# Kernel tuning notes

Hardware: AMD Instinct MI355X
Metric: run time of the kernel (lower is better)

Reference implementation:

```python
import jax, jax.numpy as jnp
import numpy as np

N_HIT = 30000   # hits per plane
N_EDGE = 90000  # Delaunay planar edges per plane (~3N)
N_SP = 30000    # spacepoints
H = 128         # hidden dim
F_IN = 4        # wire, time, integral, rms
N_CLASS = 5     # semantic classes
N_ITERS = 3     # core message-passing iterations
PLANES = ("u", "v", "y")


def setup_inputs() -> dict:
    key = jax.random.key(0)
    ks = iter(jax.random.split(key, 64))
    inp = {}
    for p in PLANES:
        inp[f"x_{p}"] = jax.random.normal(next(ks), (N_HIT, F_IN), jnp.float32)
        inp[f"edge_{p}"] = jax.random.randint(next(ks), (2, N_EDGE), 0, N_HIT)
        # row 0: hit index in plane, row 1: spacepoint index
        inp[f"nexus_{p}"] = jax.random.randint(next(ks), (2, N_SP), 0, N_HIT)
    def lin(k, i, o):
        return (jax.random.normal(k, (i, o), jnp.float32) / np.sqrt(i)).astype(jnp.float32)
    inp["W_enc"] = lin(next(ks), F_IN, H); inp["b_enc"] = jnp.zeros((H,), jnp.float32)
    inp["W_msg1"] = lin(next(ks), 2 * H, H); inp["b_msg1"] = jnp.zeros((H,), jnp.float32)
    inp["W_msg2"] = lin(next(ks), H, H); inp["b_msg2"] = jnp.zeros((H,), jnp.float32)
    inp["W_upd"] = lin(next(ks), 2 * H, H); inp["b_upd"] = jnp.zeros((H,), jnp.float32)
    inp["W_sp"] = lin(next(ks), H, H); inp["b_sp"] = jnp.zeros((H,), jnp.float32)
    inp["W_nx"] = lin(next(ks), 2 * H, H); inp["b_nx"] = jnp.zeros((H,), jnp.float32)
    inp["W_sem"] = lin(next(ks), H, N_CLASS); inp["b_sem"] = jnp.zeros((N_CLASS,), jnp.float32)
    return inp


def _segment_mean(data, ids, num):
    s = jax.ops.segment_sum(data, ids, num_segments=num)
    c = jax.ops.segment_sum(jnp.ones((ids.shape[0],), data.dtype), ids, num_segments=num)
    return s / jnp.maximum(c, 1.0)[:, None]


def _core(hs, edges, nexus, W_msg1, b_msg1, W_msg2, b_msg2, W_upd, b_upd,
          W_sp, b_sp, W_nx, b_nx):
    # --- planar convolution per plane (gather-transform-scatter) ---
    new_hs = []
    for h, e in zip(hs, edges):
        src, dst = e[0], e[1]
        m = jnp.concatenate([h[dst], h[src]], axis=-1)          # [E, 2H]
        m = jax.nn.relu(m @ W_msg1 + b_msg1) @ W_msg2 + b_msg2  # [E, H]
        agg = _segment_mean(m, dst, h.shape[0])                 # [N, H]
        upd = jax.nn.relu(jnp.concatenate([h, agg], -1) @ W_upd + b_upd)
        new_hs.append(h + upd)
    hs = new_hs
    # --- nexus convolution: planes -> spacepoints -> planes ---
    sp = jnp.zeros((N_SP, hs[0].shape[1]), hs[0].dtype)
    for h, nx in zip(hs, nexus):
        sp = sp + _segment_mean(h[nx[0]], nx[1], N_SP)
    sp = jax.nn.relu(sp @ W_sp + b_sp)                          # [N_SP, H]
    out_hs = []
    for h, nx in zip(hs, nexus):
        back = _segment_mean(sp[nx[1]], nx[0], h.shape[0])      # [N, H]
        upd = jax.nn.relu(jnp.concatenate([h, back], -1) @ W_nx + b_nx)
        out_hs.append(h + upd)
    return out_hs


def reference(x_u, x_v, x_y, edge_u, edge_v, edge_y, nexus_u, nexus_v, nexus_y,
              W_enc, b_enc, W_msg1, b_msg1, W_msg2, b_msg2, W_upd, b_upd,
              W_sp, b_sp, W_nx, b_nx, W_sem, b_sem):
    edges = (edge_u, edge_v, edge_y)
    nexus = (nexus_u, nexus_v, nexus_y)
    # encoder
    hs = [jax.nn.relu(x @ W_enc + b_enc) for x in (x_u, x_v, x_y)]
    # core message-passing iterations (planar + nexus)
    for _ in range(N_ITERS):
        hs = _core(hs, edges, nexus, W_msg1, b_msg1, W_msg2, b_msg2,
                   W_upd, b_upd, W_sp, b_sp, W_nx, b_nx)
    # semantic decoder per plane
    return tuple(h @ W_sem + b_sem for h in hs)
```

## Files before the change

### kernel.cpp

```cpp
#include <hip/hip_runtime.h>
#include <hip/hip_fp16.h>

#define N_HITS 30000
#define N_EDGES 90000
#define N_SPS 30000
#define HD 128
#define NCLS 5

#define PADM 136

typedef __attribute__((ext_vector_type(8))) _Float16 f16x8;
typedef __attribute__((ext_vector_type(4))) float floatx4;

__device__ __forceinline__ float2 h2f2(uint u) {
    union { uint u; __half2 h; } x; x.u = u;
    return __half22float2(x.h);
}
__device__ __forceinline__ uint f2h2(float a, float b) {
    union { uint u; __half2 h; } x;
    x.h = __halves2half2(__float2half(a), __float2half(b));
    return x.u;
}

__global__ void hist_all_kernel(const int* __restrict__ eu, const int* __restrict__ ev,
                                const int* __restrict__ ey, const int* __restrict__ nu,
                                const int* __restrict__ nv, const int* __restrict__ ny,
                                int* __restrict__ cnt) {
    int gid = blockIdx.x * blockDim.x + threadIdx.x;
    if (gid >= 450000) return;
    int p = gid / 150000;
    int r = gid - p * 150000;
    const int* e = (p == 0) ? eu : (p == 1) ? ev : ey;
    const int* nx = (p == 0) ? nu : (p == 1) ? nv : ny;
    if (r < N_EDGES) {
        atomicAdd(&cnt[p * 30000 + e[N_EDGES + r]], 1);
    } else if (r < N_EDGES + N_SPS) {
        int i = r - N_EDGES;
        atomicAdd(&cnt[(3 + p) * 30000 + nx[N_SPS + i]], 1);
    } else {
        int i = r - N_EDGES - N_SPS;
        atomicAdd(&cnt[(6 + p) * 30000 + nx[i]], 1);
    }
}

__launch_bounds__(1024)
__global__ void scan_kernel(const int* __restrict__ cnt, int* __restrict__ off,
                            int* __restrict__ cursor) {
    int seg = blockIdx.x;
    const int* c = cnt + seg * 30000;
    int* o = off + seg * 30001;
    int* cur = cursor + seg * 30000;
    int t = threadIdx.x;
    int base = t * 30;
    int lc[30];
    int sum = 0;
#pragma unroll
    for (int k = 0; k < 30; ++k) {
        int i = base + k;
        lc[k] = (i < 30000) ? c[i] : 0;
        sum += lc[k];
    }
    __shared__ int part[1024];
    part[t] = sum;
    __syncthreads();
    for (int d = 1; d < 1024; d <<= 1) {
        int x = (t >= d) ? part[t - d] : 0;
        __syncthreads();
        part[t] += x;
        __syncthreads();
    }
    int run = part[t] - sum;
#pragma unroll
    for (int k = 0; k < 30; ++k) {
        int i = base + k;
        if (i < 30000) { o[i] = run; cur[i] = run; run += lc[k]; }
    }
    if (t == 1023) o[30000] = part[1023];
}

__global__ void fill_kernel(const int* __restrict__ eu, const int* __restrict__ ev,
                            const int* __restrict__ ey, const int* __restrict__ nu,
                            const int* __restrict__ nv, const int* __restrict__ ny,
                            int* __restrict__ cursor, int* __restrict__ csr_e,
                            int* __restrict__ csr_s, int* __restrict__ csr_h) {
    int gid = blockIdx.x * blockDim.x + threadIdx.x;
    if (gid >= 450000) return;
    int p = gid / 150000;
    int r = gid - p * 150000;
    const int* e = (p == 0) ? eu : (p == 1) ? ev : ey;
    const int* nx = (p == 0) ? nu : (p == 1) ? nv : ny;
    if (r < N_EDGES) {
        int d = e[N_EDGES + r];
        int pos = atomicAdd(&cursor[p * 30000 + d], 1);
        csr_e[p * N_EDGES + pos] = e[r];
    } else if (r < N_EDGES + N_SPS) {
        int i = r - N_EDGES;
        int spid = nx[N_SPS + i];
        int pos = atomicAdd(&cursor[(3 + p) * 30000 + spid], 1);
        csr_s[p * N_SPS + pos] = nx[i];
    } else {
        int i = r - N_EDGES - N_SPS;
        int hit = nx[i];
        int pos = atomicAdd(&cursor[(6 + p) * 30000 + hit], 1);
        csr_h[p * N_SPS + pos] = nx[N_SPS + i];
    }
}

__device__ __forceinline__ void pack4(const float* __restrict__ W, _Float16* __restrict__ P,
                                      int idx, int koff) {
    int j = idx & 7, lane = (idx >> 3) & 63, ks = (idx >> 9) & 3, n = (idx >> 11) & 7;
    int k = ks * 32 + (lane >> 4) * 8 + j, col = n * 16 + (lane & 15);
    P[idx] = (_Float16)W[(k + koff) * 128 + col];
}
__device__ __forceinline__ void pack8(const float* __restrict__ W, _Float16* __restrict__ P, int idx) {
    int j = idx & 7, lane = (idx >> 3) & 63, ks = (idx >> 9) & 7, n = (idx >> 12) & 7;
    int k = ks * 32 + (lane >> 4) * 8 + j, col = n * 16 + (lane & 15);
    P[idx] = (_Float16)W[k * 128 + col];
}

__global__ void wprep_kernel(const float* __restrict__ W1, const float* __restrict__ W2,
                             const float* __restrict__ Wu, const float* __restrict__ Wn,
                             const float* __restrict__ Wsp, _Float16* __restrict__ packs) {
    int gid = blockIdx.x * blockDim.x + threadIdx.x;
    if (gid < 16384) { pack4(W1, packs, gid, 0); return; }
    gid -= 16384;
    if (gid < 16384) { pack4(W1, packs + 16384, gid, 128); return; }
    gid -= 16384;
    if (gid < 16384) { pack4(W2, packs + 32768, gid, 0); return; }
    gid -= 16384;
    if (gid < 32768) { pack8(Wu, packs + 49152, gid); return; }
    gid -= 32768;
    if (gid < 32768) { pack8(Wn, packs + 81920, gid); return; }
    gid -= 32768;
    if (gid < 16384) { pack4(Wsp, packs + 114688, gid, 0); }
}

__launch_bounds__(256, 4)
__global__ void enc_y_kernel(const float* __restrict__ xu, const float* __restrict__ xv,
                             const float* __restrict__ xy, const float* __restrict__ We,
                             const float* __restrict__ be, const _Float16* __restrict__ W1sP,
                             _Float16* __restrict__ h, _Float16* __restrict__ y_s) {
    __shared__ _Float16 sA[128 * PADM];
    int t = threadIdx.x;
    int n0b = blockIdx.x * 128;
    const int M = 3 * N_HITS;
    for (int i = t; i < 2048; i += 256) {
        int row = i >> 4, c = i & 15;
        int n = n0b + row; if (n >= M) n = M - 1;
        int p = n / N_HITS;
        int nn = n - p * N_HITS;
        const float* x = (p == 0) ? xu : (p == 1) ? xv : xy;
        float4 xv4 = *(const float4*)(x + nn * 4);
        union { _Float16 o8[8]; uint4 u; } outv;
#pragma unroll
        for (int j = 0; j < 8; ++j) {
            int col = c * 8 + j;
            float acc = be[col];
            acc = fmaf(xv4.x, We[0 * HD + col], acc);
            acc = fmaf(xv4.y, We[1 * HD + col], acc);
            acc = fmaf(xv4.z, We[2 * HD + col], acc);
            acc = fmaf(xv4.w, We[3 * HD + col], acc);
            outv.o8[j] = (_Float16)fmaxf(acc, 0.f);
        }
        *(uint4*)&sA[row * PADM + c * 8] = outv.u;
        if (n0b + row < M) ((uint4*)(h + (size_t)n * HD))[c] = outv.u;
    }
    __syncthreads();

    int lane = t & 63, wave = t >> 6;
    int lcol = lane & 15, quad = lane >> 4;
    int nt0 = wave * 2;
    bool odd = (lcol & 1) != 0;

    const f16x8* wp = (const f16x8*)W1sP;
    f16x8 B[2][4];
#pragma unroll
    for (int nt = 0; nt < 2; ++nt)
#pragma unroll
        for (int ks = 0; ks < 4; ++ks)
            B[nt][ks] = wp[((nt0 + nt) * 4 + ks) * 64 + lane];
    floatx4 acc[8][2];
#pragma unroll
    for (int mt = 0; mt < 8; ++mt) { acc[mt][0] = (floatx4){0,0,0,0}; acc[mt][1] = (floatx4){0,0,0,0}; }
#pragma unroll
    for (int mt = 0; mt < 8; ++mt)
#pragma unroll
        for (int ks = 0; ks < 4; ++ks) {
            f16x8 a = *(const f16x8*)&sA[(mt * 16 + lcol) * PADM + ks * 32 + quad * 8];
            acc[mt][0] = __builtin_amdgcn_mfma_f32_16x16x32_f16(a, B[0][ks], acc[mt][0], 0, 0, 0);
            acc[mt][1] = __builtin_amdgcn_mfma_f32_16x16x32_f16(a, B[1][ks], acc[mt][1], 0, 0, 0);
        }
    __syncthreads();
#pragma unroll
    for (int mt = 0; mt < 8; ++mt)
#pragma unroll
        for (int r = 0; r < 4; ++r) {
            float v0 = acc[mt][0][r], v1 = acc[mt][1][r];
            float p0 = __shfl_xor(v0, 1), p1 = __shfl_xor(v1, 1);
            float av = odd ? p1 : v0, bv = odd ? v1 : p0;
            int col = nt0 * 16 + (odd ? 15 + lcol : lcol);
            *(uint*)&sA[(mt * 16 + quad * 4 + r) * PADM + col] = f2h2(av, bv);
        }
    __syncthreads();
    for (int i = t; i < 2048; i += 256) {
        int row = i >> 4, c = i & 15;
        int n = n0b + row;
        if (n < M) ((uint4*)(y_s + (size_t)n * HD))[c] = *(uint4*)&sA[row * PADM + c * 8];
    }
}

#define ECAP 640
__launch_bounds__(256, 4)
__global__ void update_planar_kernel(_Float16* __restrict__ h, const _Float16* __restrict__ y_s,
                                     const int* __restrict__ off, const int* __restrict__ csr_e,
                                     const float* __restrict__ b1, const _Float16* __restrict__ W1dP,
                                     const _Float16* __restrict__ W2P, const float* __restrict__ b2,
                                     const _Float16* __restrict__ WuP, const float* __restrict__ bu) {
    int p = blockIdx.y;
    _Float16* hp = h + (size_t)p * N_HITS * HD;
    const _Float16* ysp = y_s + (size_t)p * N_HITS * HD;
    const int* o = off + p * 30001;
    const int* csr = csr_e + p * N_EDGES;

    __shared__ _Float16 sH[64 * PADM];
    __shared__ _Float16 sA[64 * PADM];
    __shared__ int sOff[65];
    __shared__ int sIdx[ECAP];
    int t = threadIdx.x;
    int n0b = blockIdx.x * 64;
    int lane = t & 63, wave = t >> 6;
    int lcol = lane & 15, quad = lane >> 4;
    int nt0 = wave * 2;
    bool odd = (lcol & 1) != 0;

    if (t < 65) {
        int idx = n0b + t; if (idx > N_HITS) idx = N_HITS;
        sOff[t] = o[idx];
    }
    for (int i = t; i < 1024; i += 256) {
        int row = i >> 4, c = i & 15;
        int n = n0b + row; if (n >= N_HITS) n = N_HITS - 1;
        *(uint4*)&sH[row * PADM + c * 8] = ((const uint4*)(hp + (size_t)n * HD))[c];
    }
    __syncthreads();
    int base = sOff[0];
    int total = sOff[64] - base;
    bool useL = (total <= ECAP);
    if (useL) for (int i = t; i < total; i += 256) sIdx[i] = csr[base + i];

    floatx4 yd[4][2], accU[4][2];
    {
        const f16x8* w1 = (const f16x8*)W1dP;
        const f16x8* wu = (const f16x8*)WuP;
        f16x8 B1[2][4], BU[2][4];
#pragma unroll
        for (int nt = 0; nt < 2; ++nt)
#pragma unroll
            for (int ks = 0; ks < 4; ++ks) {
                B1[nt][ks] = w1[((nt0 + nt) * 4 + ks) * 64 + lane];
                BU[nt][ks] = wu[((nt0 + nt) * 8 + ks) * 64 + lane];
            }
#pragma unroll
        for (int nt = 0; nt < 2; ++nt) {
            float bv = bu[(nt0 + nt) * 16 + lcol];
#pragma unroll
            for (int mt = 0; mt < 4; ++mt) {
                yd[mt][nt] = (floatx4){0, 0, 0, 0};
                accU[mt][nt] = (floatx4){bv, bv, bv, bv};
            }
        }
#pragma unroll
        for (int mt = 0; mt < 4; ++mt)
#pragma unroll
            for (int ks = 0; ks < 4; ++ks) {
                f16x8 a = *(const f16x8*)&sH[(mt * 16 + lcol) * PADM + ks * 32 + quad * 8];
                yd[mt][0] = __builtin_amdgcn_mfma_f32_16x16x32_f16(a, B1[0][ks], yd[mt][0], 0, 0, 0);
                yd[mt][1] = __builtin_amdgcn_mfma_f32_16x16x32_f16(a, B1[1][ks], yd[mt][1], 0, 0, 0);
                accU[mt][0] = __builtin_amdgcn_mfma_f32_16x16x32_f16(a, BU[0][ks], accU[mt][0], 0, 0, 0);
                accU[mt][1] = __builtin_amdgcn_mfma_f32_16x16x32_f16(a, BU[1][ks], accU[mt][1], 0, 0, 0);
            }
    }
#pragma unroll
    for (int mt = 0; mt < 4; ++mt)
#pragma unroll
        for (int r = 0; r < 4; ++r) {
            float v0 = yd[mt][0][r], v1 = yd[mt][1][r];
            float p0 = __shfl_xor(v0, 1), p1 = __shfl_xor(v1, 1);
            float av = odd ? p1 : v0, bv = odd ? v1 : p0;
            int col = nt0 * 16 + (odd ? 15 + lcol : lcol);
            av += b1[col]; bv += b1[col + 1];
            *(uint*)&sA[(mt * 16 + quad * 4 + r) * PADM + col] = f2h2(av, bv);
        }
    __syncthreads();
    for (int i = t; i < 1024; i += 256) {
        int row = i >> 4, c = i & 15;
        int d = n0b + row;
        int beg = 0, end = 0;
        if (d < N_HITS) { beg = sOff[row]; end = sOff[row + 1]; }
        f16x8 ydv = *(const f16x8*)&sA[row * PADM + c * 8];
        f16x8 accv = (f16x8)(_Float16)0;
        for (int k = beg; k < end; ++k) {
            int s = useL ? sIdx[k - base] : csr[k];
            f16x8 ys = *(const f16x8*)&ysp[(size_t)s * HD + c * 8];
            accv += __builtin_elementwise_max(ys + ydv, (f16x8)(_Float16)0);
        }
        _Float16 iv = (_Float16)((end > beg) ? 1.f / (float)(end - beg) : 0.f);
        accv *= iv;
        *(f16x8*)&sA[row * PADM + c * 8] = accv;
    }
    __syncthreads();
    floatx4 agg[4][2];
    {
        const f16x8* w2p = (const f16x8*)W2P;
        f16x8 B[2][4];
#pragma unroll
        for (int nt = 0; nt < 2; ++nt)
#pragma unroll
            for (int ks = 0; ks < 4; ++ks)
                B[nt][ks] = w2p[((nt0 + nt) * 4 + ks) * 64 + lane];
#pragma unroll
        for (int nt = 0; nt < 2; ++nt) {
            float bv = b2[(nt0 + nt) * 16 + lcol];
#pragma unroll
            for (int mt = 0; mt < 4; ++mt) agg[mt][nt] = (floatx4){bv, bv, bv, bv};
        }
#pragma unroll
        for (int mt = 0; mt < 4; ++mt)
#pragma unroll
            for (int ks = 0; ks < 4; ++ks) {
                f16x8 a = *(const f16x8*)&sA[(mt * 16 + lcol) * PADM + ks * 32 + quad * 8];
                agg[mt][0] = __builtin_amdgcn_mfma_f32_16x16x32_f16(a, B[0][ks], agg[mt][0], 0, 0, 0);
                agg[mt][1] = __builtin_amdgcn_mfma_f32_16x16x32_f16(a, B[1][ks], agg[mt][1], 0, 0, 0);
            }
    }
    __syncthreads();
#pragma unroll
    for (int mt = 0; mt < 4; ++mt)
#pragma unroll
        for (int r = 0; r < 4; ++r) {
            float v0 = agg[mt][0][r], v1 = agg[mt][1][r];
            float p0 = __shfl_xor(v0, 1), p1 = __shfl_xor(v1, 1);
            float av = odd ? p1 : v0, bv = odd ? v1 : p0;
            int col = nt0 * 16 + (odd ? 15 + lcol : lcol);
            *(uint*)&sA[(mt * 16 + quad * 4 + r) * PADM + col] = f2h2(av, bv);
        }
    __syncthreads();
    {
        const f16x8* wu = (const f16x8*)WuP;
        f16x8 B[2][4];
#pragma unroll
        for (int nt = 0; nt < 2; ++nt)
#pragma unroll
            for (int ks = 0; ks < 4; ++ks)
                B[nt][ks] = wu[((nt0 + nt) * 8 + 4 + ks) * 64 + lane];
#pragma unroll
        for (int mt = 0; mt < 4; ++mt)
#pragma unroll
            for (int ks = 0; ks < 4; ++ks) {
                f16x8 a = *(const f16x8*)&sA[(mt * 16 + lcol) * PADM + ks * 32 + quad * 8];
                accU[mt][0] = __builtin_amdgcn_mfma_f32_16x16x32_f16(a, B[0][ks], accU[mt][0], 0, 0, 0);
                accU[mt][1] = __builtin_amdgcn_mfma_f32_16x16x32_f16(a, B[1][ks], accU[mt][1], 0, 0, 0);
            }
    }
    __syncthreads();
#pragma unroll
    for (int mt = 0; mt < 4; ++mt)
#pragma unroll
        for (int r = 0; r < 4; ++r) {
            float v0 = fmaxf(accU[mt][0][r], 0.f), v1 = fmaxf(accU[mt][1][r], 0.f);
            float p0 = __shfl_xor(v0, 1), p1 = __shfl_xor(v1, 1);
            float av = odd ? p1 : v0, bv = odd ? v1 : p0;
            int col = nt0 * 16 + (odd ? 15 + lcol : lcol);
            uint* sp2 = (uint*)&sH[(mt * 16 + quad * 4 + r) * PADM + col];
            float2 ho = h2f2(*sp2);
            *sp2 = f2h2(ho.x + av, ho.y + bv);
        }
    __syncthreads();
    for (int i = t; i < 1024; i += 256) {
        int row = i >> 4, c = i & 15;
        int n = n0b + row;
        if (n < N_HITS) ((uint4*)(hp + (size_t)n * HD))[c] = *(uint4*)&sH[row * PADM + c * 8];
    }
}

#define SCAP 576
__launch_bounds__(256, 4)
__global__ void sp_fused_kernel(const _Float16* __restrict__ h, const int* __restrict__ off,
                                const int* __restrict__ csr_s, const _Float16* __restrict__ WspP,
                                const float* __restrict__ b, _Float16* __restrict__ spf) {
    __shared__ _Float16 sA[64 * PADM];
    __shared__ int sOff[3][65];
    __shared__ int sIdx[SCAP];
    int t = threadIdx.x;
    int n0b = blockIdx.x * 64;
    int lane = t & 63, wave = t >> 6;
    int lcol = lane & 15, quad = lane >> 4;
    int nt0 = wave * 2;
    bool odd = (lcol & 1) != 0;

    if (t < 195) {
        int p = t / 65, i = t - p * 65;
        int idx = n0b + i; if (idx > N_SPS) idx = N_SPS;
        sOff[p][i] = off[(3 + p) * 30001 + idx];
    }
    __syncthreads();
    int base0 = sOff[0][0], len0 = sOff[0][64] - base0;
    int base1 = sOff[1][0], len1 = sOff[1][64] - base1;
    int base2 = sOff[2][0], len2 = sOff[2][64] - base2;
    int ofs1 = len0, ofs2 = len0 + len1;
    bool useL = (ofs2 + len2 <= SCAP);
    if (useL) {
        for (int i = t; i < len0; i += 256) sIdx[i] = csr_s[base0 + i];
        for (int i = t; i < len1; i += 256) sIdx[ofs1 + i] = csr_s[N_SPS + base1 + i];
        for (int i = t; i < len2; i += 256) sIdx[ofs2 + i] = csr_s[2 * N_SPS + base2 + i];
    }
    __syncthreads();

    for (int i = t; i < 1024; i += 256) {
        int row = i >> 4, c = i & 15;
        int s = n0b + row;
        f16x8 tv = (f16x8)(_Float16)0;
        if (s < N_SPS) {
#pragma unroll
            for (int p = 0; p < 3; ++p) {
                int beg = sOff[p][row], end = sOff[p][row + 1];
                int bb = (p == 0) ? base0 : (p == 1) ? base1 : base2;
                int oo = (p == 0) ? 0 : (p == 1) ? ofs1 : ofs2;
                const int* csr = csr_s + p * N_SPS;
                const _Float16* hb = h + (size_t)p * N_HITS * HD;
                f16x8 sv = (f16x8)(_Float16)0;
                for (int k = beg; k < end; ++k) {
                    int hit = useL ? sIdx[oo + (k - bb)] : csr[k];
                    sv += *(const f16x8*)&hb[(size_t)hit * HD + c * 8];
                }
                _Float16 iv = (_Float16)((end > beg) ? 1.f / (float)(end - beg) : 0.f);
                tv += sv * iv;
            }
        }
        *(f16x8*)&sA[row * PADM + c * 8] = tv;
    }
    __syncthreads();

    const f16x8* wp = (const f16x8*)WspP;
    f16x8 B[2][4];
#pragma unroll
    for (int nt = 0; nt < 2; ++nt)
#pragma unroll
        for (int ks = 0; ks < 4; ++ks)
            B[nt][ks] = wp[((nt0 + nt) * 4 + ks) * 64 + lane];

    floatx4 acc[4][2];
#pragma unroll
    for (int nt = 0; nt < 2; ++nt) {
        float bv = b[(nt0 + nt) * 16 + lcol];
#pragma unroll
        for (int mt = 0; mt < 4; ++mt) acc[mt][nt] = (floatx4){bv, bv, bv, bv};
    }
#pragma unroll
    for (int mt = 0; mt < 4; ++mt)
#pragma unroll
        for (int ks = 0; ks < 4; ++ks) {
            f16x8 a = *(const f16x8*)&sA[(mt * 16 + lcol) * PADM + ks * 32 + quad * 8];
            acc[mt][0] = __builtin_amdgcn_mfma_f32_16x16x32_f16(a, B[0][ks], acc[mt][0], 0, 0, 0);
            acc[mt][1] = __builtin_amdgcn_mfma_f32_16x16x32_f16(a, B[1][ks], acc[mt][1], 0, 0, 0);
        }
    __syncthreads();
#pragma unroll
    for (int mt = 0; mt < 4; ++mt)
#pragma unroll
        for (int r = 0; r < 4; ++r) {
            float v0 = fmaxf(acc[mt][0][r], 0.f), v1 = fmaxf(acc[mt][1][r], 0.f);
            float p0 = __shfl_xor(v0, 1), p1 = __shfl_xor(v1, 1);
            float av = odd ? p1 : v0, bv = odd ? v1 : p0;
            int col = nt0 * 16 + (odd ? 15 + lcol : lcol);
            *(uint*)&sA[(mt * 16 + quad * 4 + r) * PADM + col] = f2h2(av, bv);
        }
    __syncthreads();
    for (int i = t; i < 1024; i += 256) {
        int row = i >> 4, c = i & 15;
        int n = n0b + row;
        if (n < N_SPS) ((uint4*)(spf + (size_t)n * HD))[c] = *(uint4*)&sA[row * PADM + c * 8];
    }
}

#define HCAP 320
__launch_bounds__(256, 4)
__global__ void update_y_kernel(_Float16* __restrict__ h, const _Float16* __restrict__ sp,
                                const int* __restrict__ off, const int* __restrict__ csr_h,
                                const _Float16* __restrict__ WP, const float* __restrict__ b,
                                const _Float16* __restrict__ W1sP, _Float16* __restrict__ y_s) {
    int p = blockIdx.y;
    _Float16* hp = h + (size_t)p * N_HITS * HD;
    _Float16* ysp = y_s + (size_t)p * N_HITS * HD;
    const int* o = off + (6 + p) * 30001;
    const int* csr = csr_h + p * N_SPS;

    __shared__ _Float16 sH[64 * PADM];
    __shared__ _Float16 sA[64 * PADM];
    __shared__ int sOff[65];
    __shared__ int sIdx[HCAP];
    int t = threadIdx.x;
    int n0b = blockIdx.x * 64;
    int lane = t & 63, wave = t >> 6;
    int lcol = lane & 15, quad = lane >> 4;
    int nt0 = wave * 2;
    bool odd = (lcol & 1) != 0;

    if (t < 65) {
        int idx = n0b + t; if (idx > N_HITS) idx = N_HITS;
        sOff[t] = o[idx];
    }
    for (int i = t; i < 1024; i += 256) {
        int row = i >> 4, c = i & 15;
        int n = n0b + row; if (n >= N_HITS) n = N_HITS - 1;
        *(uint4*)&sH[row * PADM + c * 8] = ((const uint4*)(hp + (size_t)n * HD))[c];
    }
    __syncthreads();
    int base = sOff[0];
    int total = sOff[64] - base;
    bool useL = (total <= HCAP);
    if (useL) for (int i = t; i < total; i += 256) sIdx[i] = csr[base + i];
    __syncthreads();

    for (int i = t; i < 1024; i += 256) {
        int row = i >> 4, c = i & 15;
        int hit = n0b + row;
        int beg = 0, end = 0;
        if (hit < N_HITS) { beg = sOff[row]; end = sOff[row + 1]; }
        f16x8 av8 = (f16x8)(_Float16)0;
        for (int k = beg; k < end; ++k) {
            int spid = useL ? sIdx[k - base] : csr[k];
            av8 += *(const f16x8*)&sp[(size_t)spid * HD + c * 8];
        }
        _Float16 iv = (_Float16)((end > beg) ? 1.f / (float)(end - beg) : 0.f);
        av8 *= iv;
        *(f16x8*)&sA[row * PADM + c * 8] = av8;
    }
    __syncthreads();
    floatx4 acc[4][2];
    {
        const f16x8* wp = (const f16x8*)WP;
        f16x8 BH[2][4], BA[2][4];
#pragma unroll
        for (int nt = 0; nt < 2; ++nt)
#pragma unroll
            for (int ks = 0; ks < 4; ++ks) {
                BH[nt][ks] = wp[((nt0 + nt) * 8 + ks) * 64 + lane];
                BA[nt][ks] = wp[((nt0 + nt) * 8 + 4 + ks) * 64 + lane];
            }
#pragma unroll
        for (int nt = 0; nt < 2; ++nt) {
            float bv = b[(nt0 + nt) * 16 + lcol];
#pragma unroll
            for (int mt = 0; mt < 4; ++mt) acc[mt][nt] = (floatx4){bv, bv, bv, bv};
        }
#pragma unroll
        for (int mt = 0; mt < 4; ++mt)
#pragma unroll
            for (int ks = 0; ks < 4; ++ks) {
                f16x8 ah = *(const f16x8*)&sH[(mt * 16 + lcol) * PADM + ks * 32 + quad * 8];
                f16x8 aa = *(const f16x8*)&sA[(mt * 16 + lcol) * PADM + ks * 32 + quad * 8];
                acc[mt][0] = __builtin_amdgcn_mfma_f32_16x16x32_f16(ah, BH[0][ks], acc[mt][0], 0, 0, 0);
                acc[mt][1] = __builtin_amdgcn_mfma_f32_16x16x32_f16(ah, BH[1][ks], acc[mt][1], 0, 0, 0);
                acc[mt][0] = __builtin_amdgcn_mfma_f32_16x16x32_f16(aa, BA[0][ks], acc[mt][0], 0, 0, 0);
                acc[mt][1] = __builtin_amdgcn_mfma_f32_16x16x32_f16(aa, BA[1][ks], acc[mt][1], 0, 0, 0);
            }
    }
    __syncthreads();
#pragma unroll
    for (int mt = 0; mt < 4; ++mt)
#pragma unroll
        for (int r = 0; r < 4; ++r) {
            float v0 = fmaxf(acc[mt][0][r], 0.f), v1 = fmaxf(acc[mt][1][r], 0.f);
            float p0 = __shfl_xor(v0, 1), p1 = __shfl_xor(v1, 1);
            float av = odd ? p1 : v0, bv = odd ? v1 : p0;
            int col = nt0 * 16 + (odd ? 15 + lcol : lcol);
            uint* sp2 = (uint*)&sH[(mt * 16 + quad * 4 + r) * PADM + col];
            float2 ho = h2f2(*sp2);
            *sp2 = f2h2(ho.x + av, ho.y + bv);
        }
    __syncthreads();
    for (int i = t; i < 1024; i += 256) {
        int row = i >> 4, c = i & 15;
        int n = n0b + row;
        if (n < N_HITS) ((uint4*)(hp + (size_t)n * HD))[c] = *(uint4*)&sH[row * PADM + c * 8];
    }
    {
        const f16x8* wyp = (const f16x8*)W1sP;
        f16x8 B[2][4];
#pragma unroll
        for (int nt = 0; nt < 2; ++nt)
#pragma unroll
            for (int ks = 0; ks < 4; ++ks)
                B[nt][ks] = wyp[((nt0 + nt) * 4 + ks) * 64 + lane];
        floatx4 yacc[4][2];
#pragma unroll
        for (int mt = 0; mt < 4; ++mt) { yacc[mt][0] = (floatx4){0,0,0,0}; yacc[mt][1] = (floatx4){0,0,0,0}; }
#pragma unroll
        for (int mt = 0; mt < 4; ++mt)
#pragma unroll
            for (int ks = 0; ks < 4; ++ks) {
                f16x8 a = *(const f16x8*)&sH[(mt * 16 + lcol) * PADM + ks * 32 + quad * 8];
                yacc[mt][0] = __builtin_amdgcn_mfma_f32_16x16x32_f16(a, B[0][ks], yacc[mt][0], 0, 0, 0);
                yacc[mt][1] = __builtin_amdgcn_mfma_f32_16x16x32_f16(a, B[1][ks], yacc[mt][1], 0, 0, 0);
            }
#pragma unroll
        for (int mt = 0; mt < 4; ++mt)
#pragma unroll
            for (int r = 0; r < 4; ++r) {
                float v0 = yacc[mt][0][r], v1 = yacc[mt][1][r];
                float p0 = __shfl_xor(v0, 1), p1 = __shfl_xor(v1, 1);
                float av = odd ? p1 : v0, bv = odd ? v1 : p0;
                int col = nt0 * 16 + (odd ? 15 + lcol : lcol);
                *(uint*)&sA[(mt * 16 + quad * 4 + r) * PADM + col] = f2h2(av, bv);
            }
    }
    __syncthreads();
    for (int i = t; i < 1024; i += 256) {
        int row = i >> 4, c = i & 15;
        int n = n0b + row;
        if (n < N_HITS) ((uint4*)(ysp + (size_t)n * HD))[c] = *(uint4*)&sA[row * PADM + c * 8];
    }
}

__global__ void dec_kernel(const _Float16* __restrict__ h, const float* __restrict__ W,
                           const float* __restrict__ b, float* __restrict__ out) {
    __shared__ float sW[640];
    __shared__ float sB[8];
    int t = threadIdx.x;
    for (int i = t; i < 640; i += 256) sW[i] = W[i];
    if (t < 5) sB[t] = b[t];
    __syncthreads();
    int n = blockIdx.x * 256 + t;
    if (n >= 3 * N_HITS) return;
    const uint4* hr = (const uint4*)(h + (size_t)n * HD);
    float a0 = sB[0], a1 = sB[1], a2 = sB[2], a3 = sB[3], a4 = sB[4];
#pragma unroll 4
    for (int q = 0; q < 16; ++q) {
        union { uint4 u; _Float16 hh[8]; } v; v.u = hr[q];
        const float* w = &sW[q * 40];
#pragma unroll
        for (int j = 0; j < 8; ++j) {
            float x = (float)v.hh[j];
            a0 = fmaf(x, w[j * 5 + 0], a0);
            a1 = fmaf(x, w[j * 5 + 1], a1);
            a2 = fmaf(x, w[j * 5 + 2], a2);
            a3 = fmaf(x, w[j * 5 + 3], a3);
            a4 = fmaf(x, w[j * 5 + 4], a4);
        }
    }
    float* oo = out + (size_t)n * NCLS;
    oo[0] = a0; oo[1] = a1; oo[2] = a2; oo[3] = a3; oo[4] = a4;
}

extern "C" void kernel_launch(void* const* d_in, const int* in_sizes, int n_in,
                              void* d_out, int out_size, void* d_ws, size_t ws_size,
                              hipStream_t stream) {
    const float* xu = (const float*)d_in[0];
    const int* eu = (const int*)d_in[1];
    const int* nu = (const int*)d_in[2];
    const float* xv = (const float*)d_in[3];
    const int* ev = (const int*)d_in[4];
    const int* nv = (const int*)d_in[5];
    const float* xy = (const float*)d_in[6];
    const int* ey = (const int*)d_in[7];
    const int* ny = (const int*)d_in[8];
    const float* W_enc = (const float*)d_in[9];
    const float* b_enc = (const float*)d_in[10];
    const float* W1 = (const float*)d_in[11];
    const float* b1 = (const float*)d_in[12];
    const float* W2 = (const float*)d_in[13];
    const float* b2 = (const float*)d_in[14];
    const float* W_upd = (const float*)d_in[15];
    const float* b_upd = (const float*)d_in[16];
    const float* W_sp = (const float*)d_in[17];
    const float* b_sp = (const float*)d_in[18];
    const float* W_nx = (const float*)d_in[19];
    const float* b_nx = (const float*)d_in[20];
    const float* W_sem = (const float*)d_in[21];
    const float* b_sem = (const float*)d_in[22];

    const size_t HN = (size_t)3 * N_HITS * HD;
    _Float16* h = (_Float16*)d_ws;
    _Float16* y_s = h + HN;
    _Float16* sp = y_s + HN;
    int* cnt = (int*)(sp + (size_t)N_SPS * HD);
    int* off = cnt + 270000;
    int* cursor = off + 270009;
    int* csr_e = cursor + 270000;
    int* csr_s = csr_e + 270000;
    int* csr_h = csr_s + 90000;
    _Float16* packs = (_Float16*)(csr_h + 90000);
    _Float16* W1dP = packs;
    _Float16* W1sP = packs + 16384;
    _Float16* W2P = packs + 32768;
    _Float16* WuP = packs + 49152;
    _Float16* WnP = packs + 81920;
    _Float16* WspP = packs + 114688;

    wprep_kernel<<<512, 256, 0, stream>>>(W1, W2, W_upd, W_nx, W_sp, packs);
    (void)hipMemsetAsync(cnt, 0, 270000 * sizeof(int), stream);
    hist_all_kernel<<<(450000 + 255) / 256, 256, 0, stream>>>(eu, ev, ey, nu, nv, ny, cnt);
    scan_kernel<<<9, 1024, 0, stream>>>(cnt, off, cursor);
    fill_kernel<<<(450000 + 255) / 256, 256, 0, stream>>>(eu, ev, ey, nu, nv, ny,
                                                          cursor, csr_e, csr_s, csr_h);

    enc_y_kernel<<<(3 * N_HITS + 127) / 128, 256, 0, stream>>>(xu, xv, xy, W_enc, b_enc,
                                                               W1sP, h, y_s);

    for (int it = 0; it < 3; ++it) {
        update_planar_kernel<<<dim3((N_HITS + 63) / 64, 3), 256, 0, stream>>>(
            h, y_s, off, csr_e, b1, W1dP, W2P, b2, WuP, b_upd);
        sp_fused_kernel<<<(N_SPS + 63) / 64, 256, 0, stream>>>(h, off, csr_s, WspP, b_sp, sp);
        update_y_kernel<<<dim3((N_HITS + 63) / 64, 3), 256, 0, stream>>>(
            h, sp, off, csr_h, WnP, b_nx, W1sP, y_s);
    }

    dec_kernel<<<(3 * N_HITS + 255) / 256, 256, 0, stream>>>(h, W_sem, b_sem, (float*)d_out);
}
```

Measured before the change: 515.7 us.

## Precompute dst-projection y_d upstream to shrink planar kernel registers and LDS

The h·W1_dst projection now runs in the encoder and update_y kernels and is written to a new y_d buffer. update_planar_kernel reads it instead of recomputing it, which drops its sH buffer and the early accumulators so it can run at higher occupancy (launch bounds raised to 5 for update_planar and 6 for sp_fused). The cost is an extra 90000x128 fp16 write per iteration plus a read, more GEMM work and syncs in update_y, and a reload of h later in the planar kernel.

```diff
diff --git a/kernel.cpp b/kernel.cpp
--- a/kernel.cpp
+++ b/kernel.cpp
@@ -138,9 +138,11 @@
 __launch_bounds__(256, 4)
 __global__ void enc_y_kernel(const float* __restrict__ xu, const float* __restrict__ xv,
                              const float* __restrict__ xy, const float* __restrict__ We,
-                             const float* __restrict__ be, const _Float16* __restrict__ W1sP,
-                             _Float16* __restrict__ h, _Float16* __restrict__ y_s) {
+                             const float* __restrict__ be, const _Float16* __restrict__ W1dP,
+                             const _Float16* __restrict__ W1sP, _Float16* __restrict__ h,
+                             _Float16* __restrict__ y_d, _Float16* __restrict__ y_s) {
     __shared__ _Float16 sA[128 * PADM];
+    __shared__ _Float16 sO[128 * PADM];
     int t = threadIdx.x;
     int n0b = blockIdx.x * 128;
     const int M = 3 * N_HITS;
@@ -172,57 +174,61 @@
     int nt0 = wave * 2;
     bool odd = (lcol & 1) != 0;
 
-    const f16x8* wp = (const f16x8*)W1sP;
-    f16x8 B[2][4];
-#pragma unroll
-    for (int nt = 0; nt < 2; ++nt)
-#pragma unroll
-        for (int ks = 0; ks < 4; ++ks)
-            B[nt][ks] = wp[((nt0 + nt) * 4 + ks) * 64 + lane];
-    floatx4 acc[8][2];
-#pragma unroll
-    for (int mt = 0; mt < 8; ++mt) { acc[mt][0] = (floatx4){0,0,0,0}; acc[mt][1] = (floatx4){0,0,0,0}; }
-#pragma unroll
-    for (int mt = 0; mt < 8; ++mt)
-#pragma unroll
-        for (int ks = 0; ks < 4; ++ks) {
-            f16x8 a = *(const f16x8*)&sA[(mt * 16 + lcol) * PADM + ks * 32 + quad * 8];
-            acc[mt][0] = __builtin_amdgcn_mfma_f32_16x16x32_f16(a, B[0][ks], acc[mt][0], 0, 0, 0);
-            acc[mt][1] = __builtin_amdgcn_mfma_f32_16x16x32_f16(a, B[1][ks], acc[mt][1], 0, 0, 0);
-        }
-    __syncthreads();
-#pragma unroll
-    for (int mt = 0; mt < 8; ++mt)
-#pragma unroll
-        for (int r = 0; r < 4; ++r) {
-            float v0 = acc[mt][0][r], v1 = acc[mt][1][r];
-            float p0 = __shfl_xor(v0, 1), p1 = __shfl_xor(v1, 1);
-            float av = odd ? p1 : v0, bv = odd ? v1 : p0;
-            int col = nt0 * 16 + (odd ? 15 + lcol : lcol);
-            *(uint*)&sA[(mt * 16 + quad * 4 + r) * PADM + col] = f2h2(av, bv);
-        }
-    __syncthreads();
-    for (int i = t; i < 2048; i += 256) {
-        int row = i >> 4, c = i & 15;
-        int n = n0b + row;
-        if (n < M) ((uint4*)(y_s + (size_t)n * HD))[c] = *(uint4*)&sA[row * PADM + c * 8];
+    for (int half = 0; half < 2; ++half) {
+        const f16x8* wp = (const f16x8*)(half == 0 ? W1dP : W1sP);
+        _Float16* out = half == 0 ? y_d : y_s;
+        f16x8 B[2][4];
+#pragma unroll
+        for (int nt = 0; nt < 2; ++nt)
+#pragma unroll
+            for (int ks = 0; ks < 4; ++ks)
+                B[nt][ks] = wp[((nt0 + nt) * 4 + ks) * 64 + lane];
+        floatx4 acc[8][2];
+#pragma unroll
+        for (int mt = 0; mt < 8; ++mt) { acc[mt][0] = (floatx4){0,0,0,0}; acc[mt][1] = (floatx4){0,0,0,0}; }
+#pragma unroll
+        for (int mt = 0; mt < 8; ++mt)
+#pragma unroll
+            for (int ks = 0; ks < 4; ++ks) {
+                f16x8 a = *(const f16x8*)&sA[(mt * 16 + lcol) * PADM + ks * 32 + quad * 8];
+                acc[mt][0] = __builtin_amdgcn_mfma_f32_16x16x32_f16(a, B[0][ks], acc[mt][0], 0, 0, 0);
+                acc[mt][1] = __builtin_amdgcn_mfma_f32_16x16x32_f16(a, B[1][ks], acc[mt][1], 0, 0, 0);
+            }
+#pragma unroll
+        for (int mt = 0; mt < 8; ++mt)
+#pragma unroll
+            for (int r = 0; r < 4; ++r) {
+                float v0 = acc[mt][0][r], v1 = acc[mt][1][r];
+                float p0 = __shfl_xor(v0, 1), p1 = __shfl_xor(v1, 1);
+                float av = odd ? p1 : v0, bv = odd ? v1 : p0;
+                int col = nt0 * 16 + (odd ? 15 + lcol : lcol);
+                *(uint*)&sO[(mt * 16 + quad * 4 + r) * PADM + col] = f2h2(av, bv);
+            }
+        __syncthreads();
+        for (int i = t; i < 2048; i += 256) {
+            int row = i >> 4, c = i & 15;
+            int n = n0b + row;
+            if (n < M) ((uint4*)(out + (size_t)n * HD))[c] = *(uint4*)&sO[row * PADM + c * 8];
+        }
+        __syncthreads();
     }
 }
 
 #define ECAP 640
-__launch_bounds__(256, 4)
-__global__ void update_planar_kernel(_Float16* __restrict__ h, const _Float16* __restrict__ y_s,
+__launch_bounds__(256, 5)
+__global__ void update_planar_kernel(_Float16* __restrict__ h, const _Float16* __restrict__ y_d,
+                                     const _Float16* __restrict__ y_s,
                                      const int* __restrict__ off, const int* __restrict__ csr_e,
-                                     const float* __restrict__ b1, const _Float16* __restrict__ W1dP,
+                                     const float* __restrict__ b1,
                                      const _Float16* __restrict__ W2P, const float* __restrict__ b2,
                                      const _Float16* __restrict__ WuP, const float* __restrict__ bu) {
     int p = blockIdx.y;
     _Float16* hp = h + (size_t)p * N_HITS * HD;
+    const _Float16* ydp = y_d + (size_t)p * N_HITS * HD;
     const _Float16* ysp = y_s + (size_t)p * N_HITS * HD;
     const int* o = off + p * 30001;
     const int* csr = csr_e + p * N_EDGES;
 
-    __shared__ _Float16 sH[64 * PADM];
     __shared__ _Float16 sA[64 * PADM];
     __shared__ int sOff[65];
     __shared__ int sIdx[ECAP];
@@ -240,58 +246,22 @@
     for (int i = t; i < 1024; i += 256) {
         int row = i >> 4, c = i & 15;
         int n = n0b + row; if (n >= N_HITS) n = N_HITS - 1;
-        *(uint4*)&sH[row * PADM + c * 8] = ((const uint4*)(hp + (size_t)n * HD))[c];
+        f16x8 yv = *(const f16x8*)&ydp[(size_t)n * HD + c * 8];
+        float4 b1a = *(const float4*)(b1 + c * 8);
+        float4 b1b = *(const float4*)(b1 + c * 8 + 4);
+        float bb[8] = {b1a.x, b1a.y, b1a.z, b1a.w, b1b.x, b1b.y, b1b.z, b1b.w};
+        f16x8 ov;
+#pragma unroll
+        for (int j = 0; j < 8; ++j) ov[j] = (_Float16)((float)yv[j] + bb[j]);
+        *(f16x8*)&sA[row * PADM + c * 8] = ov;
     }
     __syncthreads();
     int base = sOff[0];
     int total = sOff[64] - base;
     bool useL = (total <= ECAP);
     if (useL) for (int i = t; i < total; i += 256) sIdx[i] = csr[base + i];
-
-    floatx4 yd[4][2], accU[4][2];
-    {
-        const f16x8* w1 = (const f16x8*)W1dP;
-        const f16x8* wu = (const f16x8*)WuP;
-        f16x8 B1[2][4], BU[2][4];
-#pragma unroll
-        for (int nt = 0; nt < 2; ++nt)
-#pragma unroll
-            for (int ks = 0; ks < 4; ++ks) {
-                B1[nt][ks] = w1[((nt0 + nt) * 4 + ks) * 64 + lane];
-                BU[nt][ks] = wu[((nt0 + nt) * 8 + ks) * 64 + lane];
-            }
-#pragma unroll
-        for (int nt = 0; nt < 2; ++nt) {
-            float bv = bu[(nt0 + nt) * 16 + lcol];
-#pragma unroll
-            for (int mt = 0; mt < 4; ++mt) {
-                yd[mt][nt] = (floatx4){0, 0, 0, 0};
-                accU[mt][nt] = (floatx4){bv, bv, bv, bv};
-            }
-        }
-#pragma unroll
-        for (int mt = 0; mt < 4; ++mt)
-#pragma unroll
-            for (int ks = 0; ks < 4; ++ks) {
-                f16x8 a = *(const f16x8*)&sH[(mt * 16 + lcol) * PADM + ks * 32 + quad * 8];
-                yd[mt][0] = __builtin_amdgcn_mfma_f32_16x16x32_f16(a, B1[0][ks], yd[mt][0], 0, 0, 0);
-                yd[mt][1] = __builtin_amdgcn_mfma_f32_16x16x32_f16(a, B1[1][ks], yd[mt][1], 0, 0, 0);
-                accU[mt][0] = __builtin_amdgcn_mfma_f32_16x16x32_f16(a, BU[0][ks], accU[mt][0], 0, 0, 0);
-                accU[mt][1] = __builtin_amdgcn_mfma_f32_16x16x32_f16(a, BU[1][ks], accU[mt][1], 0, 0, 0);
-            }
-    }
-#pragma unroll
-    for (int mt = 0; mt < 4; ++mt)
-#pragma unroll
-        for (int r = 0; r < 4; ++r) {
-            float v0 = yd[mt][0][r], v1 = yd[mt][1][r];
-            float p0 = __shfl_xor(v0, 1), p1 = __shfl_xor(v1, 1);
-            float av = odd ? p1 : v0, bv = odd ? v1 : p0;
-            int col = nt0 * 16 + (odd ? 15 + lcol : lcol);
-            av += b1[col]; bv += b1[col + 1];
-            *(uint*)&sA[(mt * 16 + quad * 4 + r) * PADM + col] = f2h2(av, bv);
-        }
-    __syncthreads();
+    __syncthreads();
+
     for (int i = t; i < 1024; i += 256) {
         int row = i >> 4, c = i & 15;
         int d = n0b + row;
@@ -309,7 +279,7 @@
         *(f16x8*)&sA[row * PADM + c * 8] = accv;
     }
     __syncthreads();
-    floatx4 agg[4][2];
+    floatx4 acc[4][2];
     {
         const f16x8* w2p = (const f16x8*)W2P;
         f16x8 B[2][4];
@@ -322,15 +292,15 @@
         for (int nt = 0; nt < 2; ++nt) {
             float bv = b2[(nt0 + nt) * 16 + lcol];
 #pragma unroll
-            for (int mt = 0; mt < 4; ++mt) agg[mt][nt] = (floatx4){bv, bv, bv, bv};
+            for (int mt = 0; mt < 4; ++mt) acc[mt][nt] = (floatx4){bv, bv, bv, bv};
         }
 #pragma unroll
         for (int mt = 0; mt < 4; ++mt)
 #pragma unroll
             for (int ks = 0; ks < 4; ++ks) {
                 f16x8 a = *(const f16x8*)&sA[(mt * 16 + lcol) * PADM + ks * 32 + quad * 8];
-                agg[mt][0] = __builtin_amdgcn_mfma_f32_16x16x32_f16(a, B[0][ks], agg[mt][0], 0, 0, 0);
-                agg[mt][1] = __builtin_amdgcn_mfma_f32_16x16x32_f16(a, B[1][ks], agg[mt][1], 0, 0, 0);
+                acc[mt][0] = __builtin_amdgcn_mfma_f32_16x16x32_f16(a, B[0][ks], acc[mt][0], 0, 0, 0);
+                acc[mt][1] = __builtin_amdgcn_mfma_f32_16x16x32_f16(a, B[1][ks], acc[mt][1], 0, 0, 0);
             }
     }
     __syncthreads();
@@ -338,7 +308,7 @@
     for (int mt = 0; mt < 4; ++mt)
 #pragma unroll
         for (int r = 0; r < 4; ++r) {
-            float v0 = agg[mt][0][r], v1 = agg[mt][1][r];
+            float v0 = acc[mt][0][r], v1 = acc[mt][1][r];
             float p0 = __shfl_xor(v0, 1), p1 = __shfl_xor(v1, 1);
             float av = odd ? p1 : v0, bv = odd ? v1 : p0;
             int col = nt0 * 16 + (odd ? 15 + lcol : lcol);
@@ -353,13 +323,46 @@
 #pragma unroll
             for (int ks = 0; ks < 4; ++ks)
                 B[nt][ks] = wu[((nt0 + nt) * 8 + 4 + ks) * 64 + lane];
+        floatx4 tmp[4][2];
+#pragma unroll
+        for (int nt = 0; nt < 2; ++nt) {
+            float bv = bu[(nt0 + nt) * 16 + lcol];
+#pragma unroll
+            for (int mt = 0; mt < 4; ++mt) tmp[mt][nt] = (floatx4){bv, bv, bv, bv};
+        }
 #pragma unroll
         for (int mt = 0; mt < 4; ++mt)
 #pragma unroll
             for (int ks = 0; ks < 4; ++ks) {
                 f16x8 a = *(const f16x8*)&sA[(mt * 16 + lcol) * PADM + ks * 32 + quad * 8];
-                accU[mt][0] = __builtin_amdgcn_mfma_f32_16x16x32_f16(a, B[0][ks], accU[mt][0], 0, 0, 0);
-                accU[mt][1] = __builtin_amdgcn_mfma_f32_16x16x32_f16(a, B[1][ks], accU[mt][1], 0, 0, 0);
+                tmp[mt][0] = __builtin_amdgcn_mfma_f32_16x16x32_f16(a, B[0][ks], tmp[mt][0], 0, 0, 0);
+                tmp[mt][1] = __builtin_amdgcn_mfma_f32_16x16x32_f16(a, B[1][ks], tmp[mt][1], 0, 0, 0);
+            }
+#pragma unroll
+        for (int mt = 0; mt < 4; ++mt) { acc[mt][0] = tmp[mt][0]; acc[mt][1] = tmp[mt][1]; }
+    }
+    __syncthreads();
+    for (int i = t; i < 1024; i += 256) {
+        int row = i >> 4, c = i & 15;
+        int n = n0b + row; if (n >= N_HITS) n = N_HITS - 1;
+        *(uint4*)&sA[row * PADM + c * 8] = ((const uint4*)(hp + (size_t)n * HD))[c];
+    }
+    __syncthreads();
+    {
+        const f16x8* wu = (const f16x8*)WuP;
+        f16x8 B[2][4];
+#pragma unroll
+        for (int nt = 0; nt < 2; ++nt)
+#pragma unroll
+            for (int ks = 0; ks < 4; ++ks)
+                B[nt][ks] = wu[((nt0 + nt) * 8 + ks) * 64 + lane];
+#pragma unroll
+        for (int mt = 0; mt < 4; ++mt)
+#pragma unroll
+            for (int ks = 0; ks < 4; ++ks) {
+                f16x8 a = *(const f16x8*)&sA[(mt * 16 + lcol) * PADM + ks * 32 + quad * 8];
+                acc[mt][0] = __builtin_amdgcn_mfma_f32_16x16x32_f16(a, B[0][ks], acc[mt][0], 0, 0, 0);
+                acc[mt][1] = __builtin_amdgcn_mfma_f32_16x16x32_f16(a, B[1][ks], acc[mt][1], 0, 0, 0);
             }
     }
     __syncthreads();
@@ -367,11 +370,11 @@
     for (int mt = 0; mt < 4; ++mt)
 #pragma unroll
         for (int r = 0; r < 4; ++r) {
-            float v0 = fmaxf(accU[mt][0][r], 0.f), v1 = fmaxf(accU[mt][1][r], 0.f);
+            float v0 = fmaxf(acc[mt][0][r], 0.f), v1 = fmaxf(acc[mt][1][r], 0.f);
             float p0 = __shfl_xor(v0, 1), p1 = __shfl_xor(v1, 1);
             float av = odd ? p1 : v0, bv = odd ? v1 : p0;
             int col = nt0 * 16 + (odd ? 15 + lcol : lcol);
-            uint* sp2 = (uint*)&sH[(mt * 16 + quad * 4 + r) * PADM + col];
+            uint* sp2 = (uint*)&sA[(mt * 16 + quad * 4 + r) * PADM + col];
             float2 ho = h2f2(*sp2);
             *sp2 = f2h2(ho.x + av, ho.y + bv);
         }
@@ -379,12 +382,12 @@
     for (int i = t; i < 1024; i += 256) {
         int row = i >> 4, c = i & 15;
         int n = n0b + row;
-        if (n < N_HITS) ((uint4*)(hp + (size_t)n * HD))[c] = *(uint4*)&sH[row * PADM + c * 8];
+        if (n < N_HITS) ((uint4*)(hp + (size_t)n * HD))[c] = *(uint4*)&sA[row * PADM + c * 8];
     }
 }
 
 #define SCAP 576
-__launch_bounds__(256, 4)
+__launch_bounds__(256, 6)
 __global__ void sp_fused_kernel(const _Float16* __restrict__ h, const int* __restrict__ off,
                                 const int* __restrict__ csr_s, const _Float16* __restrict__ WspP,
                                 const float* __restrict__ b, _Float16* __restrict__ spf) {
@@ -488,9 +491,11 @@
 __global__ void update_y_kernel(_Float16* __restrict__ h, const _Float16* __restrict__ sp,
                                 const int* __restrict__ off, const int* __restrict__ csr_h,
                                 const _Float16* __restrict__ WP, const float* __restrict__ b,
-                                const _Float16* __restrict__ W1sP, _Float16* __restrict__ y_s) {
+                                const _Float16* __restrict__ W1dP, const _Float16* __restrict__ W1sP,
+                                _Float16* __restrict__ y_d, _Float16* __restrict__ y_s) {
     int p = blockIdx.y;
     _Float16* hp = h + (size_t)p * N_HITS * HD;
+    _Float16* ydp = y_d + (size_t)p * N_HITS * HD;
     _Float16* ysp = y_s + (size_t)p * N_HITS * HD;
     const int* o = off + (6 + p) * 30001;
     const int* csr = csr_h + p * N_SPS;
@@ -585,8 +590,9 @@
         int n = n0b + row;
         if (n < N_HITS) ((uint4*)(hp + (size_t)n * HD))[c] = *(uint4*)&sH[row * PADM + c * 8];
     }
-    {
-        const f16x8* wyp = (const f16x8*)W1sP;
+    for (int half = 0; half < 2; ++half) {
+        const f16x8* wyp = (const f16x8*)(half == 0 ? W1sP : W1dP);
+        _Float16* out = half == 0 ? ysp : ydp;
         f16x8 B[2][4];
 #pragma unroll
         for (int nt = 0; nt < 2; ++nt)
@@ -604,6 +610,7 @@
                 yacc[mt][0] = __builtin_amdgcn_mfma_f32_16x16x32_f16(a, B[0][ks], yacc[mt][0], 0, 0, 0);
                 yacc[mt][1] = __builtin_amdgcn_mfma_f32_16x16x32_f16(a, B[1][ks], yacc[mt][1], 0, 0, 0);
             }
+        __syncthreads();
 #pragma unroll
         for (int mt = 0; mt < 4; ++mt)
 #pragma unroll
@@ -614,12 +621,12 @@
                 int col = nt0 * 16 + (odd ? 15 + lcol : lcol);
                 *(uint*)&sA[(mt * 16 + quad * 4 + r) * PADM + col] = f2h2(av, bv);
             }
-    }
-    __syncthreads();
-    for (int i = t; i < 1024; i += 256) {
-        int row = i >> 4, c = i & 15;
-        int n = n0b + row;
-        if (n < N_HITS) ((uint4*)(ysp + (size_t)n * HD))[c] = *(uint4*)&sA[row * PADM + c * 8];
+        __syncthreads();
+        for (int i = t; i < 1024; i += 256) {
+            int row = i >> 4, c = i & 15;
+            int n = n0b + row;
+            if (n < N_HITS) ((uint4*)(out + (size_t)n * HD))[c] = *(uint4*)&sA[row * PADM + c * 8];
+        }
     }
 }
 
@@ -683,7 +690,8 @@
     const size_t HN = (size_t)3 * N_HITS * HD;
     _Float16* h = (_Float16*)d_ws;
     _Float16* y_s = h + HN;
-    _Float16* sp = y_s + HN;
+    _Float16* y_d = y_s + HN;
+    _Float16* sp = y_d + HN;
     int* cnt = (int*)(sp + (size_t)N_SPS * HD);
     int* off = cnt + 270000;
     int* cursor = off + 270009;
@@ -706,14 +714,14 @@
                                                           cursor, csr_e, csr_s, csr_h);
 
     enc_y_kernel<<<(3 * N_HITS + 127) / 128, 256, 0, stream>>>(xu, xv, xy, W_enc, b_enc,
-                                                               W1sP, h, y_s);
+                                                               W1dP, W1sP, h, y_d, y_s);
 
     for (int it = 0; it < 3; ++it) {
         update_planar_kernel<<<dim3((N_HITS + 63) / 64, 3), 256, 0, stream>>>(
-            h, y_s, off, csr_e, b1, W1dP, W2P, b2, WuP, b_upd);
+            h, y_d, y_s, off, csr_e, b1, W2P, b2, WuP, b_upd);
         sp_fused_kernel<<<(N_SPS + 63) / 64, 256, 0, stream>>>(h, off, csr_s, WspP, b_sp, sp);
         update_y_kernel<<<dim3((N_HITS + 63) / 64, 3), 256, 0, stream>>>(
-            h, sp, off, csr_h, WnP, b_nx, W1sP, y_s);
+            h, sp, off, csr_h, WnP, b_nx, W1dP, W1sP, y_d, y_s);
     }
 
     dec_kernel<<<(3 * N_HITS + 255) / 256, 256, 0, stream>>>(h, W_sem, b_sem, (float*)d_out);
```

Measured after the change: 514.0 us. No clear change (-0.3%).
